# Kernel tuning notes

Measured on AMD Instinct MI355X. Metric: run time of the kernel, lower is better.

Reference implementation:

```python
import jax, jax.numpy as jnp
import numpy as np

B, S, H = 2, 1024, 768
D, HID = 24, 96            # hdim_proj_dim, hdim_mlp_hidden
VIN, VHID = 3 * H, 2 * max(128, H // 2)  # concat_hadam -> 3H; out_hid = 768
ALPHA0 = 0.05              # init_gate_hdim


def setup_inputs() -> dict:
    key = jax.random.key(0)
    ks = jax.random.split(key, 10)
    sc = 0.02
    return {
        "H_j": jax.random.normal(ks[0], (B, S, H), jnp.float32),
        "H_i": jax.random.normal(ks[1], (B, S, H), jnp.float32),
        "attn_mask": jnp.ones((B, S), jnp.float32),
        "Wpj": jax.random.normal(ks[2], (H, D), jnp.float32) * sc,
        "Wpi": jax.random.normal(ks[3], (H, D), jnp.float32) * sc,
        "W1": jax.random.normal(ks[4], (4 * D, HID), jnp.float32) * sc,
        "b1": jnp.zeros((HID,), jnp.float32),
        "W2": jax.random.normal(ks[5], (HID, 1), jnp.float32) * sc,
        "b2": jnp.zeros((1,), jnp.float32),
        "Wv1": jax.random.normal(ks[6], (VIN, VHID), jnp.float32) * sc,
        "bv1": jnp.zeros((VHID,), jnp.float32),
        "Wv2": jax.random.normal(ks[7], (VHID, H), jnp.float32) * sc,
        "bv2": jnp.zeros((H,), jnp.float32),
        "alpha": jnp.float32(ALPHA0),
    }


def reference(H_j, H_i, attn_mask, Wpj, Wpi, W1, b1, W2, b2, Wv1, bv1, Wv2, bv2, alpha):
    # token projections: [B,S,D]
    Zj = H_j @ Wpj
    Zi = H_i @ Wpi
    # 4-term pair MLP, decomposed so the [B,S,S,4D] concat is never built:
    # cat([Zj_pair, Zi_pair, Zj*Zi, |Zj-Zi|]) @ W1 == sum of 4 partial products
    W1a, W1b, W1c, W1d = W1[:D], W1[D:2 * D], W1[2 * D:3 * D], W1[3 * D:]
    tj = Zj @ W1a                                   # [B,S,HID]
    ti = Zi @ W1b                                   # [B,S,HID]
    had = jnp.einsum('bsd,btd,dh->bsth', Zj, Zi, W1c)          # [B,S,S,HID]
    diff = jnp.abs(Zj[:, :, None, :] - Zi[:, None, :, :]) @ W1d  # [B,S,S,HID]
    h = jax.nn.relu(tj[:, :, None, :] + ti[:, None, :, :] + had + diff + b1)
    logits = (h @ W2)[..., 0] + b2[0]               # [B,S,S]
    # additive mask on key axis (torch: (1-mask)*finfo.min)
    logits = logits + (1.0 - attn_mask[:, None, :]) * jnp.finfo(logits.dtype).min
    probs = jax.nn.softmax(logits, axis=-1)
    ctx = jnp.einsum('bst,bth->bsh', probs, H_i)    # context over H_i
    # value fusion: concat_hadam -> [ctx, H_j, ctx*H_j]
    msg_in = jnp.concatenate([ctx, H_j, ctx * H_j], axis=-1)
    msg = jax.nn.relu(msg_in @ Wv1 + bv1) @ Wv2 + bv2
    return alpha * msg  # dropout is identity at eval
```

## Files before the change

kernel.cpp:

```cpp
#include <hip/hip_runtime.h>
#include <math.h>

#define BB   2
#define SS   1024
#define HH   768
#define DD   24
#define HIDD 96
#define VINN 2304
#define VHIDD 768
#define NRR  2048

typedef __attribute__((ext_vector_type(8))) short short8;
typedef __attribute__((ext_vector_type(4))) float floatx4;

static __device__ inline unsigned short f2bf(float x) {
    unsigned int u = __float_as_uint(x);
    u = (u + 0x7FFFu + ((u >> 16) & 1u)) >> 16;
    return (unsigned short)u;
}
static __device__ inline unsigned int pack2(float a, float b) {
    unsigned int r;
    asm("v_cvt_pk_bf16_f32 %0, %1, %2" : "=v"(r) : "v"(a), "v"(b));
    return r;
}

static __device__ inline void gl16(const unsigned short* g, unsigned short* l) {
    __builtin_amdgcn_global_load_lds(
        (const __attribute__((address_space(1))) unsigned int*)g,
        (__attribute__((address_space(3))) unsigned int*)l,
        16, 0, 0);
}

__global__ __launch_bounds__(256) void k_zproj(
    const float* __restrict__ Hj, const float* __restrict__ Hi,
    const float* __restrict__ Wpj, const float* __restrict__ Wpi,
    unsigned* __restrict__ Zjp, unsigned* __restrict__ Zip)
{
    __shared__ __align__(16) unsigned short sAz[64][72];
    __shared__ __align__(16) unsigned short sBTz[32][72];
    int tid = threadIdx.x;
    int w = tid >> 6, lane = tid & 63;
    int quad = lane >> 4, col = lane & 15;
    int m0 = blockIdx.x * 64;
    bool isJ = (m0 < NRR);
    const float* src = isJ ? Hj : Hi;
    const float* Wp  = isJ ? Wpj : Wpi;
    unsigned* Zp     = isJ ? Zjp : Zip;
    int rowbase = isJ ? m0 : (m0 - NRR);

    floatx4 acc[2];
    acc[0] = (floatx4){0.f,0.f,0.f,0.f};
    acc[1] = (floatx4){0.f,0.f,0.f,0.f};

    for (int kb = 0; kb < HH; kb += 64) {
        #pragma unroll
        for (int i = 0; i < 4; ++i) {
            int f4 = tid + i*256;
            int r = f4 >> 4, c4 = f4 & 15;
            float4 v = *(const float4*)(src + (size_t)(rowbase + r)*HH + kb + c4*4);
            uint2 pkt; pkt.x = pack2(v.x, v.y); pkt.y = pack2(v.z, v.w);
            *(uint2*)&sAz[r][c4*4] = pkt;
        }
        {
            const float* wsrc = Wp + (size_t)kb*DD;
            #pragma unroll
            for (int i = 0; i < 6; ++i) {
                int idx = tid + i*256;
                int k = idx / DD, n = idx % DD;
                sBTz[n][k] = f2bf(wsrc[idx]);
            }
        }
        __syncthreads();
        #pragma unroll
        for (int kt = 0; kt < 2; ++kt) {
            short8 av = *(const short8*)&sAz[w*16 + col][kt*32 + quad*8];
            #pragma unroll
            for (int nt = 0; nt < 2; ++nt) {
                short8 bv = *(const short8*)&sBTz[nt*16 + col][kt*32 + quad*8];
                acc[nt] = __builtin_amdgcn_mfma_f32_16x16x32_bf16(av, bv, acc[nt], 0, 0, 0);
            }
        }
        __syncthreads();
    }
    #pragma unroll
    for (int nt = 0; nt < 2; ++nt) {
        #pragma unroll
        for (int r = 0; r < 4; ++r) {
            float v = acc[nt][r];
            float vn = __shfl_xor(v, 1, 64);
            int n = nt*16 + col;
            if (!(col & 1) && n < DD) {
                int m = w*16 + quad*4 + r;
                Zp[(size_t)(rowbase + m)*12 + (n >> 1)] = pack2(v, vn);
            }
        }
    }
}

#define LSTR 72
#define TC 64
#define NC (SS/TC)
__global__ __launch_bounds__(256) void k_attn(
    const unsigned* __restrict__ Zjp, const unsigned* __restrict__ Zip,
    const float* __restrict__ W1, const float* __restrict__ b1,
    const float* __restrict__ W2,
    const float* __restrict__ mask, unsigned short* __restrict__ probs,
    const float* __restrict__ Hi, const float* __restrict__ Wv1,
    const float* __restrict__ Wv2,
    unsigned short* __restrict__ Wv1T, unsigned short* __restrict__ Wv2T,
    unsigned short* __restrict__ HiT)
{
    int tid = threadIdx.x;
    __shared__ __align__(16) unsigned short sAB[2][TC*LSTR];
    __shared__ __align__(16) float sLog[SS];
    __shared__ unsigned sZjp[12];
    __shared__ float sW2[HIDD];
    __shared__ float sRed[4];
    unsigned short* sABf = &sAB[0][0];

    if (blockIdx.x >= NRR) {
        int b2 = blockIdx.x - NRR;
        const float* in; unsigned short* out; int R, C, r0, c0;
        if (b2 < 1728) {
            in = Wv1; out = Wv1T; R = VINN; C = VHIDD;
            c0 = (b2 % 24) * 32; r0 = (b2 / 24) * 32;
        } else if (b2 < 2304) {
            int t = b2 - 1728;
            in = Wv2; out = Wv2T; R = VHIDD; C = HH;
            c0 = (t % 24) * 32; r0 = (t / 24) * 32;
        } else {
            int t = b2 - 2304;
            int z = t / 768; t %= 768;
            in = Hi + (size_t)z*SS*HH; out = HiT + (size_t)z*HH*SS;
            R = SS; C = HH;
            c0 = (t % 24) * 32; r0 = (t / 24) * 32;
        }
        float* tile = (float*)sABf;
        int tc = tid & 31, tr = tid >> 5;
        #pragma unroll
        for (int i = 0; i < 4; ++i)
            tile[(tr + i*8)*33 + tc] = in[(size_t)(r0 + tr + i*8)*C + c0 + tc];
        __syncthreads();
        #pragma unroll
        for (int i = 0; i < 4; ++i)
            out[(size_t)(c0 + tr + i*8)*R + r0 + tc] = f2bf(tile[tc*33 + tr + i*8]);
        return;
    }

    int row = blockIdx.x;
    int b = row >> 10;
    int lane = tid & 63, wv = tid >> 6;
    int quad = lane >> 4, col = lane & 15;

    if (tid < 12) sZjp[tid] = Zjp[(size_t)row*12 + tid];
    if (tid < HIDD) sW2[tid] = W2[tid];
    __syncthreads();

    if (tid < HIDD) {
        int h = tid;
        float zj[24];
        #pragma unroll
        for (int u = 0; u < 12; ++u) {
            unsigned z = sZjp[u];
            zj[2*u]   = __uint_as_float(z << 16);
            zj[2*u+1] = __uint_as_float(z & 0xffff0000u);
        }
        float tj = b1[h];
        #pragma unroll
        for (int d = 0; d < DD; ++d) tj = fmaf(zj[d], W1[d*HIDD + h], tj);
        unsigned short* rowp = sABf + h*LSTR;
        #pragma unroll
        for (int d = 0; d < DD; ++d)
            rowp[d] = f2bf(fmaf(zj[d], W1[(48+d)*HIDD + h], W1[(24+d)*HIDD + h]));
        #pragma unroll
        for (int d = 0; d < DD; ++d)
            rowp[24+d] = f2bf(W1[(72+d)*HIDD + h]);
        rowp[48] = f2bf(tj);
        #pragma unroll
        for (int k = 49; k < 64; ++k) rowp[k] = 0;
    }
    __syncthreads();

    short8 bfr[6][2];
    #pragma unroll
    for (int nf = 0; nf < 6; ++nf)
        #pragma unroll
        for (int kt = 0; kt < 2; ++kt)
            bfr[nf][kt] = *(const short8*)&sABf[(nf*16 + col)*LSTR + kt*32 + quad*8];
    float4 w2q[6];
    #pragma unroll
    for (int nf = 0; nf < 6; ++nf)
        w2q[nf] = *(const float4*)&sW2[nf*16 + quad*4];
    __syncthreads();

    if (lane < 32) {
        int bf = lane >> 4, r = wv*16 + (lane & 15);
        unsigned short* rowp = &sAB[bf][r*LSTR];
        uint4 w0; w0.x = 0x3F80u; w0.y = 0; w0.z = 0; w0.w = 0;
        *(uint4*)&rowp[48] = w0;
        uint4 zz; zz.x = 0; zz.y = 0; zz.z = 0; zz.w = 0;
        *(uint4*)&rowp[56] = zz;
    }

    int t_loc = tid >> 2, ss = tid & 3;
    const unsigned* zbase = Zip + (size_t)(b << 10) * 12;

    float zalo[3], zahi[3];
    #pragma unroll
    for (int u = 0; u < 3; ++u) {
        unsigned za = sZjp[3*ss + u];
        zalo[u] = __uint_as_float(za << 16);
        zahi[u] = __uint_as_float(za & 0xffff0000u);
    }

    auto issue = [&](int chunk, uint4 &cp, unsigned (&mz)[3]) {
        int t = chunk*TC + t_loc;
        const unsigned* zr = zbase + (size_t)t*12;
        if (ss < 3) cp = *(const uint4*)(zr + 4*ss);
        #pragma unroll
        for (int u = 0; u < 3; ++u) mz[u] = zr[3*ss + u];
    };
    auto packw = [&](int bf, const uint4 &cp, const unsigned (&mz)[3]) {
        unsigned short* rowp = &sAB[bf][t_loc*LSTR];
        if (ss < 3) *(uint4*)&rowp[8*ss] = cp;
        #pragma unroll
        for (int u = 0; u < 3; ++u) {
            unsigned zb = mz[u];
            float blo = __uint_as_float(zb << 16);
            float bhi = __uint_as_float(zb & 0xffff0000u);
            float dlo = fabsf(zalo[u] - blo);
            float dhi = fabsf(zahi[u] - bhi);
            *(unsigned*)&rowp[24 + 6*ss + 2*u] = pack2(dlo, dhi);
        }
    };
    auto mfma_fold = [&](int chunk, int cur) {
        int arow = wv*16 + col;
        short8 av0 = *(const short8*)&sAB[cur][arow*LSTR + quad*8];
        short8 av1 = *(const short8*)&sAB[cur][arow*LSTR + 32 + quad*8];
        float s0 = 0.f;
        __builtin_amdgcn_s_setprio(1);
        #pragma unroll
        for (int hf = 0; hf < 6; ++hf) {
            floatx4 a0 = {0.f,0.f,0.f,0.f};
            a0 = __builtin_amdgcn_mfma_f32_16x16x32_bf16(bfr[hf][0], av0, a0, 0, 0, 0);
            a0 = __builtin_amdgcn_mfma_f32_16x16x32_bf16(bfr[hf][1], av1, a0, 0, 0, 0);
            float w2v[4] = {w2q[hf].x, w2q[hf].y, w2q[hf].z, w2q[hf].w};
            #pragma unroll
            for (int r = 0; r < 4; ++r)
                s0 = fmaf(fmaxf(a0[r], 0.f), w2v[r], s0);
        }
        __builtin_amdgcn_s_setprio(0);
        s0 += __shfl_xor(s0, 16, 64);
        s0 += __shfl_xor(s0, 32, 64);
        if (lane < 16)
            sLog[chunk*TC + wv*16 + lane] = s0;
    };

    uint4 cpA, cpB; unsigned mzA[3], mzB[3];
    issue(0, cpA, mzA);
    issue(1, cpB, mzB);

    #pragma unroll
    for (int cc = 0; cc < NC; cc += 2) {
        packw(0, cpA, mzA);
        if (cc + 2 < NC) issue(cc + 2, cpA, mzA);
        mfma_fold(cc, 0);
        packw(1, cpB, mzB);
        if (cc + 3 < NC) issue(cc + 3, cpB, mzB);
        mfma_fold(cc + 1, 1);
    }
    __syncthreads();

    float lv[4];
    #pragma unroll
    for (int i = 0; i < 4; ++i) {
        int t = tid + i*256;
        lv[i] = sLog[t] + (1.0f - mask[(size_t)(b<<10) + t]) * (-3.402823466e+38f);
    }
    float m = fmaxf(fmaxf(lv[0], lv[1]), fmaxf(lv[2], lv[3]));
    #pragma unroll
    for (int off = 32; off; off >>= 1) m = fmaxf(m, __shfl_down(m, off, 64));
    if (lane == 0) sRed[wv] = m;
    __syncthreads();
    float M = fmaxf(fmaxf(sRed[0], sRed[1]), fmaxf(sRed[2], sRed[3]));
    float e[4]; float ssum = 0.f;
    #pragma unroll
    for (int i = 0; i < 4; ++i) { e[i] = expf(lv[i] - M); ssum += e[i]; }
    #pragma unroll
    for (int off = 32; off; off >>= 1) ssum += __shfl_down(ssum, off, 64);
    __syncthreads();
    if (lane == 0) sRed[wv] = ssum;
    __syncthreads();
    float inv = 1.0f / (sRed[0] + sRed[1] + sRed[2] + sRed[3]);
    #pragma unroll
    for (int i = 0; i < 4; ++i)
        probs[(size_t)row*SS + tid + i*256] = f2bf(e[i] * inv);
}

template<int MODE>
__global__ __launch_bounds__(256) void k_mgemm_nf(
    const unsigned short* __restrict__ A,
    const unsigned short* __restrict__ BT,
    const float* __restrict__ bias,
    const float* __restrict__ Hj,
    const float* __restrict__ alpha_p,
    void* __restrict__ Cout,
    int K, int bt_bstride)
{
    __shared__ __align__(16) unsigned short sA[64*64];
    __shared__ __align__(16) unsigned short sB[32*64];
    int tid = threadIdx.x;
    int w = tid >> 6, lane = tid & 63;
    int quad = lane >> 4, col = lane & 15;

    int nwgx = gridDim.x;
    int bid  = blockIdx.y * nwgx + blockIdx.x;
    int q    = (nwgx * gridDim.y) >> 3;
    int swz  = (bid & 7) * q + (bid >> 3);
    int n0 = (swz % nwgx) * 32, m0 = (swz / nwgx) * 64;

    int nk = K >> 6;
    const unsigned short* Bb = BT + (size_t)(m0 >> 10) * bt_bstride;

    int srow = lane >> 3;
    int skc  = (lane & 7) * 8;

    floatx4 acc[2];
    acc[0] = (floatx4){0.f,0.f,0.f,0.f};
    acc[1] = (floatx4){0.f,0.f,0.f,0.f};

    for (int kb = 0; kb < nk; ++kb) {
        int kofs = kb*64;
        gl16(A  + (size_t)(m0 + w*16     + srow)*K + kofs + skc, &sA[(w*16)*64]);
        gl16(A  + (size_t)(m0 + w*16 + 8 + srow)*K + kofs + skc, &sA[(w*16 + 8)*64]);
        gl16(Bb + (size_t)(n0 + w*8      + srow)*K + kofs + skc, &sB[(w*8)*64]);
        __syncthreads();
        #pragma unroll
        for (int kt = 0; kt < 2; ++kt) {
            short8 av = *(const short8*)&sA[(w*16 + col)*64 + kt*32 + quad*8];
            #pragma unroll
            for (int nf = 0; nf < 2; ++nf) {
                short8 bv = *(const short8*)&sB[(nf*16 + col)*64 + kt*32 + quad*8];
                acc[nf] = __builtin_amdgcn_mfma_f32_16x16x32_bf16(av, bv, acc[nf], 0, 0, 0);
            }
        }
        __syncthreads();
    }

    float alpha = (MODE == 2) ? alpha_p[0] : 1.0f;
    #pragma unroll
    for (int nf = 0; nf < 2; ++nf) {
        int n = n0 + nf*16 + col;
        #pragma unroll
        for (int r = 0; r < 4; ++r) {
            int m = w*16 + quad*4 + r;
            size_t g = (size_t)(m0 + m);
            float v = acc[nf][r];
            if (MODE == 0) {
                float hj = Hj[g*HH + n];
                unsigned short* msgin = (unsigned short*)Cout;
                msgin[g*VINN + n]        = f2bf(v);
                msgin[g*VINN + HH + n]   = f2bf(hj);
                msgin[g*VINN + 2*HH + n] = f2bf(v*hj);
            } else if (MODE == 1) {
                ((unsigned short*)Cout)[g*VHIDD + n] =
                    f2bf(fmaxf(v + bias[n], 0.f));
            } else {
                ((float*)Cout)[g*HH + n] = alpha*(v + bias[n]);
            }
        }
    }
}

extern "C" void kernel_launch(void* const* d_in, const int* in_sizes, int n_in,
                              void* d_out, int out_size, void* d_ws, size_t ws_size,
                              hipStream_t stream)
{
    const float* Hj   = (const float*)d_in[0];
    const float* Hi   = (const float*)d_in[1];
    const float* mask = (const float*)d_in[2];
    const float* Wpj  = (const float*)d_in[3];
    const float* Wpi  = (const float*)d_in[4];
    const float* W1   = (const float*)d_in[5];
    const float* b1   = (const float*)d_in[6];
    const float* W2   = (const float*)d_in[7];
    const float* Wv1  = (const float*)d_in[9];
    const float* bv1  = (const float*)d_in[10];
    const float* Wv2  = (const float*)d_in[11];
    const float* bv2  = (const float*)d_in[12];
    const float* alpha = (const float*)d_in[13];
    float* out = (float*)d_out;

    const int NR = NRR;
    char* p = (char*)d_ws;
    auto alloc = [&](size_t bytes) {
        char* r = p; p += (bytes + 255) & ~(size_t)255; return r;
    };
    unsigned* Zjp          = (unsigned*)alloc((size_t)NR*12*4);
    unsigned* Zip          = (unsigned*)alloc((size_t)NR*12*4);
    unsigned short* probsb = (unsigned short*)alloc((size_t)NR*SS*2);
    unsigned short* HiT    = (unsigned short*)alloc((size_t)BB*HH*SS*2);
    unsigned short* Wv1T   = (unsigned short*)alloc((size_t)VHIDD*VINN*2);
    unsigned short* Wv2T   = (unsigned short*)alloc((size_t)HH*VHIDD*2);
    unsigned short* msginb = (unsigned short*)alloc((size_t)NR*VINN*2);
    unsigned short* Y1b    = (unsigned short*)alloc((size_t)NR*VHIDD*2);

    k_zproj<<<2*NR/64, 256, 0, stream>>>(Hj, Hi, Wpj, Wpi, Zjp, Zip);

    k_attn<<<NR + 1728 + 576 + 1536, 256, 0, stream>>>(
        Zjp, Zip, W1, b1, W2, mask, probsb,
        Hi, Wv1, Wv2, Wv1T, Wv2T, HiT);

    k_mgemm_nf<0><<<dim3(HH/32, NR/64), 256, 0, stream>>>(
        probsb, HiT, nullptr, Hj, alpha, msginb, SS, HH*SS);

    k_mgemm_nf<1><<<dim3(VHIDD/32, NR/64), 256, 0, stream>>>(
        msginb, Wv1T, bv1, nullptr, alpha, Y1b, VINN, 0);

    k_mgemm_nf<2><<<dim3(HH/32, NR/64), 256, 0, stream>>>(
        Y1b, Wv2T, bv2, nullptr, alpha, out, VHIDD, 0);
}
```

Measured before the change: 188.6 us.

## Double-buffer per-wave LDS tiles in value MLP GEMM and drop block barriers

Each wave now stages its own private A rows and a full private copy of the B tile into double-buffered LDS. The next k-block's global-to-LDS loads are issued before the current block's MFMAs, and vmcnt waits replace the two __syncthreads per iteration. This is meant to overlap load latency with compute and remove block-wide synchronisation. In exchange, B-tile global traffic per wave rises fourfold and LDS use grows, which can lower occupancy. Correctness relies on each wave only reading LDS written by its own loads.

```diff
diff --git a/kernel.cpp b/kernel.cpp
--- a/kernel.cpp
+++ b/kernel.cpp
@@ -307,8 +307,8 @@
     void* __restrict__ Cout,
     int K, int bt_bstride)
 {
-    __shared__ __align__(16) unsigned short sA[64*64];
-    __shared__ __align__(16) unsigned short sB[32*64];
+    __shared__ __align__(16) unsigned short sA[4][2][16*64];
+    __shared__ __align__(16) unsigned short sB[4][2][32*64];
     int tid = threadIdx.x;
     int w = tid >> 6, lane = tid & 63;
     int quad = lane >> 4, col = lane & 15;
@@ -329,22 +329,35 @@
     acc[0] = (floatx4){0.f,0.f,0.f,0.f};
     acc[1] = (floatx4){0.f,0.f,0.f,0.f};
 
+    auto stage = [&](int kb, int p) {
+        int kofs = kb*64;
+        gl16(A + (size_t)(m0 + w*16     + srow)*K + kofs + skc, &sA[w][p][0]);
+        gl16(A + (size_t)(m0 + w*16 + 8 + srow)*K + kofs + skc, &sA[w][p][8*64]);
+        #pragma unroll
+        for (int i = 0; i < 4; ++i)
+            gl16(Bb + (size_t)(n0 + i*8 + srow)*K + kofs + skc, &sB[w][p][i*8*64]);
+    };
+
+    stage(0, 0);
     for (int kb = 0; kb < nk; ++kb) {
-        int kofs = kb*64;
-        gl16(A  + (size_t)(m0 + w*16     + srow)*K + kofs + skc, &sA[(w*16)*64]);
-        gl16(A  + (size_t)(m0 + w*16 + 8 + srow)*K + kofs + skc, &sA[(w*16 + 8)*64]);
-        gl16(Bb + (size_t)(n0 + w*8      + srow)*K + kofs + skc, &sB[(w*8)*64]);
-        __syncthreads();
+        int p = kb & 1;
+        if (kb + 1 < nk) {
+            stage(kb + 1, p ^ 1);
+            asm volatile("s_waitcnt vmcnt(6)" ::: "memory");
+        } else {
+            asm volatile("s_waitcnt vmcnt(0)" ::: "memory");
+        }
+        __builtin_amdgcn_sched_barrier(0);
         #pragma unroll
         for (int kt = 0; kt < 2; ++kt) {
-            short8 av = *(const short8*)&sA[(w*16 + col)*64 + kt*32 + quad*8];
+            short8 av = *(const short8*)&sA[w][p][col*64 + kt*32 + quad*8];
             #pragma unroll
             for (int nf = 0; nf < 2; ++nf) {
-                short8 bv = *(const short8*)&sB[(nf*16 + col)*64 + kt*32 + quad*8];
+                short8 bv = *(const short8*)&sB[w][p][(nf*16 + col)*64 + kt*32 + quad*8];
                 acc[nf] = __builtin_amdgcn_mfma_f32_16x16x32_bf16(av, bv, acc[nf], 0, 0, 0);
             }
         }
-        __syncthreads();
+        __builtin_amdgcn_sched_barrier(0);
     }
 
     float alpha = (MODE == 2) ? alpha_p[0] : 1.0f;
```

Result: no change. 185.6 us (-1.6%).
